# Performance work log

Measured on AMD Instinct MI355X. Metric: run time of the kernel, lower is better.

The kernel has to match this reference:

```python
import jax, jax.numpy as jnp
import numpy as np

B, C, H, E, V = 64, 200, 1024, 1024, 50257
NEG_INF = -100000.0


def setup_inputs() -> dict:
    key = jax.random.key(0)
    ks = jax.random.split(key, 16)
    p = 1.0 / np.sqrt(H)
    inp = {
        "input": jax.random.normal(ks[0], (B, 1, E), jnp.float32),
        "hidden": jax.random.normal(ks[1], (1, B, H), jnp.float32),
        "list_context_hidden": jax.random.normal(ks[2], (C, B, H), jnp.float32),
        "context_hiddens": jax.random.normal(ks[3], (B, C, H), jnp.float32),
        "topic_vector": jax.random.normal(ks[4], (B, 1, H), jnp.float32),
        "pad_matrix": jax.random.randint(ks[5], (B, C), 0, 2) > 0,
        # attention params
        "dyna_W": jax.random.normal(ks[6], (H, H), jnp.float32) * p,
        "dyna_U": jax.random.normal(ks[7], (H, H), jnp.float32) * p,
        "dyna_v": jax.random.normal(ks[8], (H, 1), jnp.float32) * p,
        # GRU params (torch layout: W_ih (3H, in), W_hh (3H, H))
        "W_ih": jax.random.normal(ks[9], (3 * H, 2 * H + E), jnp.float32) * p,
        "W_hh": jax.random.normal(ks[10], (3 * H, H), jnp.float32) * p,
        "b_ih": jax.random.normal(ks[11], (3 * H,), jnp.float32) * p,
        "b_hh": jax.random.normal(ks[12], (3 * H,), jnp.float32) * p,
        # output projection
        "W_out": jax.random.normal(ks[13], (V, H), jnp.float32) * p,
        "b_out": jax.random.normal(ks[14], (V,), jnp.float32) * p,
    }
    return inp


def _gru_step(x, h, W_ih, W_hh, b_ih, b_hh):
    # x: (B, in), h: (B, H) -> h': (B, H); torch GRUCell math
    gi = x @ W_ih.T + b_ih            # (B, 3H)
    gh = h @ W_hh.T + b_hh            # (B, 3H)
    r = jax.nn.sigmoid(gi[:, :H] + gh[:, :H])
    z = jax.nn.sigmoid(gi[:, H:2 * H] + gh[:, H:2 * H])
    n = jnp.tanh(gi[:, 2 * H:] + r * gh[:, 2 * H:])
    return (1.0 - z) * n + z * h


def reference(input, hidden, list_context_hidden, context_hiddens, topic_vector,
              pad_matrix, dyna_W, dyna_U, dyna_v, W_ih, W_hh, b_ih, b_hh,
              W_out, b_out):
    h0 = hidden[0]                                         # (B, H)
    # additive attention, vectorized over the C contexts
    q = h0 @ dyna_W                                        # (B, H)
    k = jnp.einsum('cbh,hk->cbk', list_context_hidden, dyna_U)  # (C, B, H)
    scores = jnp.tanh(q[None, :, :] + k) @ dyna_v          # (C, B, 1)
    scores = scores[..., 0].T                              # (B, C)
    scores = jnp.where(pad_matrix, NEG_INF, scores)
    attn = jax.nn.softmax(scores, axis=1)                  # (B, C)
    applied = jnp.einsum('bc,bch->bh', attn, context_hiddens)  # (B, H)
    # GRU over a single step
    x = jnp.concatenate([input[:, 0], topic_vector[:, 0], applied], axis=1)  # (B, E+2H)
    h_new = _gru_step(x, h0, W_ih, W_hh, b_ih, b_hh)       # (B, H)
    logits = h_new @ W_out.T + b_out                       # (B, V)
    out = jax.nn.log_softmax(logits, axis=1)
    return out, h_new[None]
```

## Files before the change

### kernel.cpp

```cpp
#include <hip/hip_runtime.h>
#include <hip/hip_bf16.h>
#include <math.h>

constexpr int Bsz = 64, Cctx = 200, Hdim = 1024, Vv = 50257;
constexpr float NEG_INF_V = -100000.0f;

typedef __attribute__((ext_vector_type(8))) short s16x8;
typedef __attribute__((ext_vector_type(4))) float fx4;
typedef unsigned int u32;

__device__ __forceinline__ unsigned short f2bf(float f) {
  unsigned int u = __builtin_bit_cast(unsigned int, f);
  unsigned int r = (u + 0x7fffu + ((u >> 16) & 1u)) >> 16;
  return (unsigned short)r;
}

__device__ __forceinline__ float fast_tanh(float x) {
  float e2 = __expf(2.f * x);
  return 1.f - 2.f / (e2 + 1.f);
}

__device__ __forceinline__ void gl_lds16(const unsigned short* g, unsigned short* l) {
  __builtin_amdgcn_global_load_lds(
      (const __attribute__((address_space(1))) u32*)g,
      (__attribute__((address_space(3))) u32*)l, 16, 0, 0);
}

__global__ __launch_bounds__(256)
void gemm_att(const unsigned short* __restrict__ Ab, const unsigned short* __restrict__ Bb,
              const float* __restrict__ qmat, const float* __restrict__ vvec,
              float* __restrict__ part_sc) {
  __shared__ unsigned short As[2][128 * 64];
  __shared__ unsigned short Bs[2][128 * 64];
  int f = blockIdx.x + blockIdx.y * 8;
  int xcd = f & 7, jj = f >> 3;
  int my = xcd + 8 * (jj % 13), mx = jj / 13;
  if (my >= 100) return;
  const int bm0 = my * 128, bn0 = mx * 128;
  const int tid = threadIdx.x, lane = tid & 63, wid = tid >> 6;
  const int wm0 = (wid >> 1) * 64, wn0 = (wid & 1) * 64;
  const int ar = lane & 15, q4 = lane >> 4;
  const int sw = ar & 7;

  auto STAGE = [&](int buf, int kt) {
    #pragma unroll
    for (int i = 0; i < 4; ++i) {
      int s = tid + i * 256;
      int row = s >> 3;
      int sc = ((s & 7) ^ (row & 7)) * 8;
      gl_lds16(&Ab[(size_t)(bm0 + row) * Hdim + kt + sc], &As[buf][s * 8]);
    }
    #pragma unroll
    for (int i = 0; i < 4; ++i) {
      int s = tid + i * 256;
      int row = s >> 3;
      int sc = ((s & 7) ^ (row & 7)) * 8;
      gl_lds16(&Bb[(size_t)(bn0 + row) * Hdim + kt + sc], &Bs[buf][s * 8]);
    }
  };

  fx4 acc[4][4] = {};
  STAGE(0, 0);
  __syncthreads();
  int buf = 0;

  for (int t = 0; t < 16; ++t) {
    if (t < 15) STAGE(buf ^ 1, (t + 1) * 64);
    asm volatile("" ::: "memory");
    #pragma unroll
    for (int kk = 0; kk < 2; ++kk) {
      s16x8 a[4], b[4];
      #pragma unroll
      for (int i = 0; i < 4; ++i)
        a[i] = *reinterpret_cast<const s16x8*>(
            &As[buf][(wm0 + i * 16 + ar) * 64 + (((kk * 4 + q4) ^ sw) * 8)]);
      #pragma unroll
      for (int j2 = 0; j2 < 4; ++j2)
        b[j2] = *reinterpret_cast<const s16x8*>(
            &Bs[buf][(wn0 + j2 * 16 + ar) * 64 + (((kk * 4 + q4) ^ sw) * 8)]);
      #pragma unroll
      for (int i = 0; i < 4; ++i)
        #pragma unroll
        for (int j2 = 0; j2 < 4; ++j2)
          acc[i][j2] = __builtin_amdgcn_mfma_f32_16x16x32_bf16(a[i], b[j2], acc[i][j2], 0, 0, 0);
    }
    __syncthreads();
    buf ^= 1;
  }

  const int rg = q4 * 4, cg = ar;
  #pragma unroll
  for (int i = 0; i < 4; ++i) {
    #pragma unroll
    for (int p = 0; p < 4; ++p) {
      int mg = bm0 + wm0 + i * 16 + rg + p;
      int brow = mg & 63;
      float rs = 0.f;
      #pragma unroll
      for (int j2 = 0; j2 < 4; ++j2) {
        int ng = bn0 + wn0 + j2 * 16 + cg;
        float t = fast_tanh(acc[i][j2][p] + qmat[brow * Hdim + ng]);
        rs += t * vvec[ng];
      }
      rs += __shfl_xor(rs, 1); rs += __shfl_xor(rs, 2);
      rs += __shfl_xor(rs, 4); rs += __shfl_xor(rs, 8);
      if (cg == 0) part_sc[mx * 12800 + brow * Cctx + (mg >> 6)] = rs;
    }
  }
}

__device__ __forceinline__ void stream_body(const unsigned short* ap, const float* bp,
                                            int stride, int extent, fx4 acc[4]) {
  float4 b0 = *reinterpret_cast<const float4*>(bp);
  float4 b1 = *reinterpret_cast<const float4*>(bp + 4);
  float4 b2 = *reinterpret_cast<const float4*>(bp + 32);
  float4 b3 = *reinterpret_cast<const float4*>(bp + 36);
  for (int kt = 0; kt < extent; kt += 64) {
    float4 c0 = b0, c1 = b1, c2 = b2, c3 = b3;
    if (kt + 64 < extent) {
      b0 = *reinterpret_cast<const float4*>(bp + kt + 64);
      b1 = *reinterpret_cast<const float4*>(bp + kt + 68);
      b2 = *reinterpret_cast<const float4*>(bp + kt + 96);
      b3 = *reinterpret_cast<const float4*>(bp + kt + 100);
    }
    s16x8 bf0, bf1;
    bf0[0] = (short)f2bf(c0.x); bf0[1] = (short)f2bf(c0.y);
    bf0[2] = (short)f2bf(c0.z); bf0[3] = (short)f2bf(c0.w);
    bf0[4] = (short)f2bf(c1.x); bf0[5] = (short)f2bf(c1.y);
    bf0[6] = (short)f2bf(c1.z); bf0[7] = (short)f2bf(c1.w);
    bf1[0] = (short)f2bf(c2.x); bf1[1] = (short)f2bf(c2.y);
    bf1[2] = (short)f2bf(c2.z); bf1[3] = (short)f2bf(c2.w);
    bf1[4] = (short)f2bf(c3.x); bf1[5] = (short)f2bf(c3.y);
    bf1[6] = (short)f2bf(c3.z); bf1[7] = (short)f2bf(c3.w);
    #pragma unroll
    for (int i = 0; i < 4; ++i) {
      s16x8 af = *reinterpret_cast<const s16x8*>(ap + (size_t)i * 16 * stride + kt);
      acc[i] = __builtin_amdgcn_mfma_f32_16x16x32_bf16(af, bf0, acc[i], 0, 0, 0);
    }
    #pragma unroll
    for (int i = 0; i < 4; ++i) {
      s16x8 af = *reinterpret_cast<const s16x8*>(ap + (size_t)i * 16 * stride + kt + 32);
      acc[i] = __builtin_amdgcn_mfma_f32_16x16x32_bf16(af, bf1, acc[i], 0, 0, 0);
    }
  }
}

template<int EPI>
__global__ __launch_bounds__(64)
void stream_gemm(const unsigned short* __restrict__ Ab,
                 const float* __restrict__ Bm, int N, int K,
                 const float* __restrict__ bias, float* __restrict__ Cout) {
  const int lane = threadIdx.x;
  const int n0 = blockIdx.x * 16;
  const int c = lane & 15, qq = lane >> 4;
  const int brow = min(n0 + c, N - 1);
  fx4 acc[4] = {};
  stream_body(Ab + (size_t)c * K + qq * 8, Bm + (size_t)brow * K + qq * 8, K, K, acc);
  const int n = n0 + c;
  if (n < N) {
    float bv = (EPI == 2) ? bias[n] : 0.f;
    #pragma unroll
    for (int i = 0; i < 4; ++i)
      #pragma unroll
      for (int p = 0; p < 4; ++p)
        Cout[(size_t)(i * 16 + qq * 4 + p) * N + n] = acc[i][p] + bv;
  }
}

__global__ __launch_bounds__(64)
void qgh_gemm(const unsigned short* __restrict__ h0b, const float* __restrict__ Wt,
              const float* __restrict__ Whh, const float* __restrict__ bhh,
              float* __restrict__ q, float* __restrict__ gh) {
  const int lane = threadIdx.x;
  const int gw = blockIdx.x;
  const bool isq = gw < 64;
  const int n0 = isq ? gw * 16 : (gw - 64) * 16;
  const int N = isq ? 1024 : 3072;
  const float* B = isq ? Wt : Whh;
  const int c = lane & 15, qq = lane >> 4;
  fx4 acc[4] = {};
  stream_body(h0b + (size_t)c * 1024 + qq * 8, B + (size_t)(n0 + c) * 1024 + qq * 8,
              1024, 1024, acc);
  const int n = n0 + c;
  float bv = isq ? 0.f : bhh[n];
  float* C = isq ? q : gh;
  #pragma unroll
  for (int i = 0; i < 4; ++i)
    #pragma unroll
    for (int p = 0; p < 4; ++p)
      C[(size_t)(i * 16 + qq * 4 + p) * N + n] = acc[i][p] + bv;
}

__global__ __launch_bounds__(64)
void gi_split(const unsigned short* __restrict__ xb, const float* __restrict__ Wih,
              float* __restrict__ part) {
  const int lane = threadIdx.x;
  const int t = blockIdx.x;
  const int w = blockIdx.y;
  const int c = lane & 15, qq = lane >> 4;
  constexpr int K = 3072, CH = 768;
  fx4 acc[4] = {};
  stream_body(xb + (size_t)c * K + w * CH + qq * 8,
              Wih + (size_t)(t * 16 + c) * K + w * CH + qq * 8, K, CH, acc);
  float* po = part + (size_t)w * 64 * 3072;
  const int n = t * 16 + c;
  #pragma unroll
  for (int i = 0; i < 4; ++i)
    #pragma unroll
    for (int p = 0; p < 4; ++p)
      po[(size_t)(i * 16 + qq * 4 + p) * 3072 + n] = acc[i][p];
}

__global__ __launch_bounds__(256)
void prep(const float* __restrict__ dW, const float* __restrict__ dU,
          const float* __restrict__ h0, float* __restrict__ Wt,
          unsigned short* __restrict__ ub, unsigned short* __restrict__ h0b) {
  const int z = blockIdx.z;
  const int tx = threadIdx.x & 31, ty = threadIdx.x >> 5;
  if (z < 2) {
    __shared__ float t[32][33];
    const float* in = z ? dU : dW;
    int bx = blockIdx.x * 32, by = blockIdx.y * 32;
    #pragma unroll
    for (int r = 0; r < 32; r += 8) t[ty + r][tx] = in[(size_t)(by + ty + r) * 1024 + bx + tx];
    __syncthreads();
    if (z == 0) {
      #pragma unroll
      for (int r = 0; r < 32; r += 8) Wt[(size_t)(bx + ty + r) * 1024 + by + tx] = t[tx][ty + r];
    } else {
      #pragma unroll
      for (int r = 0; r < 32; r += 8) ub[(size_t)(bx + ty + r) * 1024 + by + tx] = f2bf(t[tx][ty + r]);
    }
  } else {
    if (blockIdx.y) return;
    size_t i = (size_t)(blockIdx.x * 256 + threadIdx.x) * 8;
    float4 a = *reinterpret_cast<const float4*>(h0 + i);
    float4 b = *reinterpret_cast<const float4*>(h0 + i + 4);
    s16x8 h;
    h[0] = (short)f2bf(a.x); h[1] = (short)f2bf(a.y); h[2] = (short)f2bf(a.z); h[3] = (short)f2bf(a.w);
    h[4] = (short)f2bf(b.x); h[5] = (short)f2bf(b.y); h[6] = (short)f2bf(b.z); h[7] = (short)f2bf(b.w);
    *reinterpret_cast<s16x8*>(h0b + i) = h;
  }
}

__global__ void conv_bf16(const float* __restrict__ in, unsigned short* __restrict__ out) {
  size_t i = (size_t)(blockIdx.x * 256 + threadIdx.x) * 8;
  float4 a = *reinterpret_cast<const float4*>(in + i);
  float4 b = *reinterpret_cast<const float4*>(in + i + 4);
  s16x8 h;
  h[0] = (short)f2bf(a.x); h[1] = (short)f2bf(a.y); h[2] = (short)f2bf(a.z); h[3] = (short)f2bf(a.w);
  h[4] = (short)f2bf(b.x); h[5] = (short)f2bf(b.y); h[6] = (short)f2bf(b.z); h[7] = (short)f2bf(b.w);
  *reinterpret_cast<s16x8*>(out + i) = h;
}

__global__ __launch_bounds__(256)
void softmax_applied(const float* __restrict__ part_sc, const int* __restrict__ pad,
                     const float* __restrict__ ch, float* __restrict__ part) {
  const int g = blockIdx.x, b = blockIdx.y, t = threadIdx.x;
  const int lane = t & 63, w = t >> 6;
  __shared__ float at[256];
  __shared__ float red[8];
  float sv = 0.f, v = -3.4e38f;
  if (t < Cctx) {
    float s8 = 0.f;
    #pragma unroll
    for (int mx = 0; mx < 8; ++mx) s8 += part_sc[mx * 12800 + b * Cctx + t];
    sv = pad[b * Cctx + t] ? NEG_INF_V : s8;
    v = sv;
  }
  #pragma unroll
  for (int o = 1; o < 64; o <<= 1) v = fmaxf(v, __shfl_xor(v, o));
  if (lane == 0) red[w] = v;
  __syncthreads();
  float m = fmaxf(fmaxf(red[0], red[1]), fmaxf(red[2], red[3]));
  float e = (t < Cctx) ? expf(sv - m) : 0.f;
  float s = e;
  #pragma unroll
  for (int o = 1; o < 64; o <<= 1) s += __shfl_xor(s, o);
  if (lane == 0) red[4 + w] = s;
  __syncthreads();
  float tot = red[4] + red[5] + red[6] + red[7];
  at[t] = e / tot;
  __syncthreads();
  const int h = t * 4;
  float4 a4 = make_float4(0.f, 0.f, 0.f, 0.f);
  for (int c2 = g * 25; c2 < g * 25 + 25; ++c2) {
    float a = at[c2];
    float4 vv = *reinterpret_cast<const float4*>(&ch[((size_t)b * Cctx + c2) * Hdim + h]);
    a4.x += a * vv.x; a4.y += a * vv.y; a4.z += a * vv.z; a4.w += a * vv.w;
  }
  *reinterpret_cast<float4*>(&part[((size_t)b * 8 + g) * Hdim + h]) = a4;
}

__global__ void build_xb(const float* __restrict__ inp, const float* __restrict__ topic,
                         const float* __restrict__ part, unsigned short* __restrict__ xb) {
  int j = blockIdx.x * 256 + threadIdx.x;
  int b = blockIdx.y;
  float v;
  if (j < 1024) v = inp[b * 1024 + j];
  else if (j < 2048) v = topic[b * 1024 + (j - 1024)];
  else {
    const float* pp = &part[(size_t)b * 8 * Hdim + (j - 2048)];
    v = 0.f;
    #pragma unroll
    for (int g = 0; g < 8; ++g) v += pp[g * Hdim];
  }
  xb[(size_t)b * 3072 + j] = f2bf(v);
}

__global__ void gru_gate(const float* __restrict__ pgi, const float* __restrict__ bih,
                         const float* __restrict__ gh, const float* __restrict__ h0,
                         float* __restrict__ out_h, unsigned short* __restrict__ hnb) {
  int idx = blockIdx.x * 256 + threadIdx.x;
  int b = idx >> 10, j = idx & 1023;
  float gr = bih[j], gz = bih[1024 + j], gn = bih[2048 + j];
  const float* pb = pgi + (size_t)b * 3072;
  #pragma unroll
  for (int w = 0; w < 4; ++w) {
    const float* pw = pb + (size_t)w * 64 * 3072;
    gr += pw[j]; gz += pw[1024 + j]; gn += pw[2048 + j];
  }
  const float* ghb = gh + (size_t)b * 3072;
  float r = 1.f / (1.f + expf(-(gr + ghb[j])));
  float z = 1.f / (1.f + expf(-(gz + ghb[1024 + j])));
  float n = tanhf(gn + r * ghb[2048 + j]);
  float h = (1.f - z) * n + z * h0[idx];
  out_h[idx] = h;
  hnb[idx] = f2bf(h);
}

__global__ __launch_bounds__(256)
void lse_part(const float* __restrict__ out, float* __restrict__ pm, float* __restrict__ ps) {
  const int g = blockIdx.x, b = blockIdx.y, t = threadIdx.x;
  const int lane = t & 63, w = t >> 6;
  __shared__ float red[8];
  const float* row = out + (size_t)b * Vv;
  float m = -3.4e38f;
  for (int i = g * 256 + t; i < Vv; i += 2048) m = fmaxf(m, row[i]);
  #pragma unroll
  for (int o = 1; o < 64; o <<= 1) m = fmaxf(m, __shfl_xor(m, o));
  if (lane == 0) red[w] = m;
  __syncthreads();
  float mm = fmaxf(fmaxf(red[0], red[1]), fmaxf(red[2], red[3]));
  float s = 0.f;
  for (int i = g * 256 + t; i < Vv; i += 2048) s += expf(row[i] - mm);
  #pragma unroll
  for (int o = 1; o < 64; o <<= 1) s += __shfl_xor(s, o);
  if (lane == 0) red[4 + w] = s;
  __syncthreads();
  if (t == 0) {
    pm[b * 8 + g] = mm;
    ps[b * 8 + g] = red[4] + red[5] + red[6] + red[7];
  }
}

__global__ __launch_bounds__(256)
void lse_sub(float* __restrict__ out, const float* __restrict__ pm,
             const float* __restrict__ ps) {
  const int b = blockIdx.y;
  float M = -3.4e38f;
  #pragma unroll
  for (int g = 0; g < 8; ++g) M = fmaxf(M, pm[b * 8 + g]);
  float S = 0.f;
  #pragma unroll
  for (int g = 0; g < 8; ++g) S += ps[b * 8 + g] * expf(pm[b * 8 + g] - M);
  float lse = M + logf(S);
  int i = blockIdx.x * 256 + threadIdx.x;
  if (i < Vv) out[(size_t)b * Vv + i] -= lse;
}

extern "C" void kernel_launch(void* const* d_in, const int* in_sizes, int n_in,
                              void* d_out, int out_size, void* d_ws, size_t ws_size,
                              hipStream_t stream) {
  const float* input  = (const float*)d_in[0];
  const float* hidden = (const float*)d_in[1];
  const float* lch    = (const float*)d_in[2];
  const float* ch     = (const float*)d_in[3];
  const float* topic  = (const float*)d_in[4];
  const int*   pad    = (const int*)d_in[5];
  const float* dyna_W = (const float*)d_in[6];
  const float* dyna_U = (const float*)d_in[7];
  const float* dyna_v = (const float*)d_in[8];
  const float* W_ih   = (const float*)d_in[9];
  const float* W_hh   = (const float*)d_in[10];
  const float* b_ih   = (const float*)d_in[11];
  const float* b_hh   = (const float*)d_in[12];
  const float* W_out  = (const float*)d_in[13];
  const float* b_out  = (const float*)d_in[14];

  float* out   = (float*)d_out;
  float* out_h = out + (size_t)Bsz * Vv;

  float* p = (float*)d_ws;
  float* Wt      = p; p += 1024 * 1024;
  float* q       = p; p += Bsz * Hdim;
  float* part_sc = p; p += 8 * Bsz * Cctx;
  float* part_ap = p; p += Bsz * 8 * Hdim;
  float* gh      = p; p += Bsz * 3072;
  float* part_gi = p; p += 4 * Bsz * 3072;
  float* pm      = p; p += Bsz * 8;
  float* ps      = p; p += Bsz * 8;
  unsigned short* up = (unsigned short*)p;
  unsigned short* ub  = up; up += 1024 * 1024;
  unsigned short* lb  = up; up += (size_t)Cctx * Bsz * Hdim;
  unsigned short* h0b = up; up += Bsz * Hdim;
  unsigned short* hnb = up; up += Bsz * Hdim;
  unsigned short* xb  = up; up += Bsz * 3072;

  prep<<<dim3(32, 32, 3), 256, 0, stream>>>(dyna_W, dyna_U, hidden, Wt, ub, h0b);
  conv_bf16<<<(Cctx * Bsz * Hdim) / 2048, 256, 0, stream>>>(lch, lb);

  qgh_gemm<<<256, 64, 0, stream>>>(h0b, Wt, W_hh, b_hh, q, gh);

  gemm_att<<<dim3(8, 104), 256, 0, stream>>>(lb, ub, q, dyna_v, part_sc);

  softmax_applied<<<dim3(8, Bsz), 256, 0, stream>>>(part_sc, pad, ch, part_ap);
  build_xb<<<dim3(12, Bsz), 256, 0, stream>>>(input, topic, part_ap, xb);

  gi_split<<<dim3(192, 4), 64, 0, stream>>>(xb, W_ih, part_gi);

  gru_gate<<<(Bsz * Hdim) / 256, 256, 0, stream>>>(part_gi, b_ih, gh, hidden, out_h, hnb);

  stream_gemm<2><<<(Vv + 15) / 16, 64, 0, stream>>>(hnb, W_out, Vv, Hdim, b_out, out);

  lse_part<<<dim3(8, Bsz), 256, 0, stream>>>(out, pm, ps);
  lse_sub<<<dim3((Vv + 255) / 256, Bsz), 256, 0, stream>>>(out, pm, ps);
}
```

Measured before the change: 241.6 us.

## Keep 64-column dyna_U slice resident in LDS and stream A operand from global

The attention GEMM now makes each block load a full 64x1024 bf16 slice of dyna_U into LDS once (128 KB, XOR-swizzled). It then loops over M tiles, reading the list_context_hidden operand straight from global memory into registers with two-step prefetch. This replaces the double-buffered 128x128 tiling that re-staged both operands through LDS. Splitting N into 16 parts doubles the score partials, so the softmax kernel now sums 16 of them. Only 256 blocks run, each using 128 KB of LDS, so occupancy is low and A-operand latency may be poorly hidden.

```diff
diff --git a/kernel.cpp b/kernel.cpp
--- a/kernel.cpp
+++ b/kernel.cpp
@@ -20,91 +20,69 @@
   return 1.f - 2.f / (e2 + 1.f);
 }
 
-__device__ __forceinline__ void gl_lds16(const unsigned short* g, unsigned short* l) {
-  __builtin_amdgcn_global_load_lds(
-      (const __attribute__((address_space(1))) u32*)g,
-      (__attribute__((address_space(3))) u32*)l, 16, 0, 0);
-}
-
 __global__ __launch_bounds__(256)
 void gemm_att(const unsigned short* __restrict__ Ab, const unsigned short* __restrict__ Bb,
               const float* __restrict__ qmat, const float* __restrict__ vvec,
               float* __restrict__ part_sc) {
-  __shared__ unsigned short As[2][128 * 64];
-  __shared__ unsigned short Bs[2][128 * 64];
-  int f = blockIdx.x + blockIdx.y * 8;
-  int xcd = f & 7, jj = f >> 3;
-  int my = xcd + 8 * (jj % 13), mx = jj / 13;
-  if (my >= 100) return;
-  const int bm0 = my * 128, bn0 = mx * 128;
+  __shared__ unsigned short Bs[64 * 1024];
+  const int mc = blockIdx.x;
+  const int np = blockIdx.y;
+  const int n0 = np * 64;
   const int tid = threadIdx.x, lane = tid & 63, wid = tid >> 6;
-  const int wm0 = (wid >> 1) * 64, wn0 = (wid & 1) * 64;
   const int ar = lane & 15, q4 = lane >> 4;
-  const int sw = ar & 7;
-
-  auto STAGE = [&](int buf, int kt) {
-    #pragma unroll
-    for (int i = 0; i < 4; ++i) {
-      int s = tid + i * 256;
-      int row = s >> 3;
-      int sc = ((s & 7) ^ (row & 7)) * 8;
-      gl_lds16(&Ab[(size_t)(bm0 + row) * Hdim + kt + sc], &As[buf][s * 8]);
-    }
-    #pragma unroll
-    for (int i = 0; i < 4; ++i) {
-      int s = tid + i * 256;
-      int row = s >> 3;
-      int sc = ((s & 7) ^ (row & 7)) * 8;
-      gl_lds16(&Bb[(size_t)(bn0 + row) * Hdim + kt + sc], &Bs[buf][s * 8]);
-    }
-  };
-
-  fx4 acc[4][4] = {};
-  STAGE(0, 0);
-  __syncthreads();
-  int buf = 0;
-
-  for (int t = 0; t < 16; ++t) {
-    if (t < 15) STAGE(buf ^ 1, (t + 1) * 64);
-    asm volatile("" ::: "memory");
-    #pragma unroll
-    for (int kk = 0; kk < 2; ++kk) {
-      s16x8 a[4], b[4];
-      #pragma unroll
-      for (int i = 0; i < 4; ++i)
-        a[i] = *reinterpret_cast<const s16x8*>(
-            &As[buf][(wm0 + i * 16 + ar) * 64 + (((kk * 4 + q4) ^ sw) * 8)]);
-      #pragma unroll
-      for (int j2 = 0; j2 < 4; ++j2)
-        b[j2] = *reinterpret_cast<const s16x8*>(
-            &Bs[buf][(wn0 + j2 * 16 + ar) * 64 + (((kk * 4 + q4) ^ sw) * 8)]);
-      #pragma unroll
-      for (int i = 0; i < 4; ++i)
-        #pragma unroll
-        for (int j2 = 0; j2 < 4; ++j2)
-          acc[i][j2] = __builtin_amdgcn_mfma_f32_16x16x32_bf16(a[i], b[j2], acc[i][j2], 0, 0, 0);
-    }
-    __syncthreads();
-    buf ^= 1;
-  }
-
-  const int rg = q4 * 4, cg = ar;
-  #pragma unroll
-  for (int i = 0; i < 4; ++i) {
-    #pragma unroll
-    for (int p = 0; p < 4; ++p) {
-      int mg = bm0 + wm0 + i * 16 + rg + p;
-      int brow = mg & 63;
-      float rs = 0.f;
+
+  #pragma unroll
+  for (int it = 0; it < 32; ++it) {
+    int flat = tid + it * 256;
+    int row = flat >> 7, c16 = flat & 127;
+    s16x8 v = *reinterpret_cast<const s16x8*>(&Bb[(size_t)(n0 + row) * 1024 + c16 * 8]);
+    *reinterpret_cast<s16x8*>(&Bs[row * 1024 + ((c16 ^ (row & 7)) << 3)]) = v;
+  }
+  __syncthreads();
+
+  const int swz = ar & 7;
+
+  for (int mt = mc; mt < 100; mt += 16) {
+    const unsigned short* a0p = Ab + (size_t)(mt * 128 + wid * 32 + ar) * 1024 + q4 * 8;
+    const unsigned short* a1p = a0p + 16 * 1024;
+    fx4 acc[2][4] = {};
+    s16x8 c0 = *reinterpret_cast<const s16x8*>(a0p);
+    s16x8 c1 = *reinterpret_cast<const s16x8*>(a1p);
+    s16x8 n0a = *reinterpret_cast<const s16x8*>(a0p + 32);
+    s16x8 n1a = *reinterpret_cast<const s16x8*>(a1p + 32);
+    #pragma unroll 4
+    for (int k = 0; k < 32; ++k) {
+      s16x8 f0 = c0, f1 = c1;
+      c0 = n0a; c1 = n1a;
+      if (k + 2 < 32) {
+        n0a = *reinterpret_cast<const s16x8*>(a0p + (k + 2) * 32);
+        n1a = *reinterpret_cast<const s16x8*>(a1p + (k + 2) * 32);
+      }
       #pragma unroll
       for (int j2 = 0; j2 < 4; ++j2) {
-        int ng = bn0 + wn0 + j2 * 16 + cg;
-        float t = fast_tanh(acc[i][j2][p] + qmat[brow * Hdim + ng]);
-        rs += t * vvec[ng];
+        s16x8 b = *reinterpret_cast<const s16x8*>(
+            &Bs[(j2 * 16 + ar) * 1024 + (((k * 4 + q4) ^ swz) << 3)]);
+        acc[0][j2] = __builtin_amdgcn_mfma_f32_16x16x32_bf16(f0, b, acc[0][j2], 0, 0, 0);
+        acc[1][j2] = __builtin_amdgcn_mfma_f32_16x16x32_bf16(f1, b, acc[1][j2], 0, 0, 0);
       }
-      rs += __shfl_xor(rs, 1); rs += __shfl_xor(rs, 2);
-      rs += __shfl_xor(rs, 4); rs += __shfl_xor(rs, 8);
-      if (cg == 0) part_sc[mx * 12800 + brow * Cctx + (mg >> 6)] = rs;
+    }
+    #pragma unroll
+    for (int i = 0; i < 2; ++i) {
+      #pragma unroll
+      for (int p = 0; p < 4; ++p) {
+        int mg = mt * 128 + wid * 32 + i * 16 + q4 * 4 + p;
+        int brow = mg & 63;
+        float rs = 0.f;
+        #pragma unroll
+        for (int j2 = 0; j2 < 4; ++j2) {
+          int ng = n0 + j2 * 16 + ar;
+          float t = fast_tanh(acc[i][j2][p] + qmat[brow * Hdim + ng]);
+          rs += t * vvec[ng];
+        }
+        rs += __shfl_xor(rs, 1); rs += __shfl_xor(rs, 2);
+        rs += __shfl_xor(rs, 4); rs += __shfl_xor(rs, 8);
+        if (ar == 0) part_sc[np * 12800 + brow * Cctx + (mg >> 6)] = rs;
+      }
     }
   }
 }
@@ -264,7 +242,7 @@
   if (t < Cctx) {
     float s8 = 0.f;
     #pragma unroll
-    for (int mx = 0; mx < 8; ++mx) s8 += part_sc[mx * 12800 + b * Cctx + t];
+    for (int mx = 0; mx < 16; ++mx) s8 += part_sc[mx * 12800 + b * Cctx + t];
     sv = pad[b * Cctx + t] ? NEG_INF_V : s8;
     v = sv;
   }
@@ -394,7 +372,7 @@
   float* p = (float*)d_ws;
   float* Wt      = p; p += 1024 * 1024;
   float* q       = p; p += Bsz * Hdim;
-  float* part_sc = p; p += 8 * Bsz * Cctx;
+  float* part_sc = p; p += 16 * Bsz * Cctx;
   float* part_ap = p; p += Bsz * 8 * Hdim;
   float* gh      = p; p += Bsz * 3072;
   float* part_gi = p; p += 4 * Bsz * 3072;
@@ -412,7 +390,7 @@
 
   qgh_gemm<<<256, 64, 0, stream>>>(h0b, Wt, W_hh, b_hh, q, gh);
 
-  gemm_att<<<dim3(8, 104), 256, 0, stream>>>(lb, ub, q, dyna_v, part_sc);
+  gemm_att<<<dim3(16, 16), 256, 0, stream>>>(lb, ub, q, dyna_v, part_sc);
 
   softmax_applied<<<dim3(8, Bsz), 256, 0, stream>>>(part_sc, pad, ch, part_ap);
   build_xb<<<dim3(12, Bsz), 256, 0, stream>>>(input, topic, part_ap, xb);
```

After: 278.1 us. 15.1% more time.

## Use explicit vmcnt waits in attention GEMM and fuse log-softmax kernels

Applied to the files above, without the earlier changes.

The attention GEMM pipeline now waits with explicit s_waitcnt vmcnt counts and raw s_barrier calls instead of __syncthreads. This lets the prefetch of the next tile stay in flight while the current tile is consumed. The two log-sum-exp kernels are merged into one 1024-thread block per row that computes max, sum and the subtraction in a single launch. The merge drops a launch and the partial buffers, but leaves only 64 blocks to cover the whole GPU, which may underuse bandwidth.

```diff
diff --git a/kernel.cpp b/kernel.cpp
--- a/kernel.cpp
+++ b/kernel.cpp
@@ -61,12 +61,19 @@
 
   fx4 acc[4][4] = {};
   STAGE(0, 0);
-  __syncthreads();
+  asm volatile("s_waitcnt vmcnt(0)" ::: "memory");
+  __builtin_amdgcn_s_barrier();
   int buf = 0;
 
   for (int t = 0; t < 16; ++t) {
-    if (t < 15) STAGE(buf ^ 1, (t + 1) * 64);
-    asm volatile("" ::: "memory");
+    if (t < 15) {
+      STAGE(buf ^ 1, (t + 1) * 64);
+      asm volatile("s_waitcnt vmcnt(8)" ::: "memory");
+    } else {
+      asm volatile("s_waitcnt vmcnt(0)" ::: "memory");
+    }
+    __builtin_amdgcn_s_barrier();
+    __builtin_amdgcn_sched_barrier(0);
     #pragma unroll
     for (int kk = 0; kk < 2; ++kk) {
       s16x8 a[4], b[4];
@@ -84,7 +91,7 @@
         for (int j2 = 0; j2 < 4; ++j2)
           acc[i][j2] = __builtin_amdgcn_mfma_f32_16x16x32_bf16(a[i], b[j2], acc[i][j2], 0, 0, 0);
     }
-    __syncthreads();
+    __builtin_amdgcn_s_barrier();
     buf ^= 1;
   }
 
@@ -329,44 +336,32 @@
   hnb[idx] = f2bf(h);
 }
 
-__global__ __launch_bounds__(256)
-void lse_part(const float* __restrict__ out, float* __restrict__ pm, float* __restrict__ ps) {
-  const int g = blockIdx.x, b = blockIdx.y, t = threadIdx.x;
-  const int lane = t & 63, w = t >> 6;
-  __shared__ float red[8];
-  const float* row = out + (size_t)b * Vv;
+__global__ __launch_bounds__(1024)
+void lse_fused(float* __restrict__ out) {
+  const int b = blockIdx.x, t = threadIdx.x, lane = t & 63, w = t >> 6;
+  __shared__ float red[16];
+  float* row = out + (size_t)b * Vv;
   float m = -3.4e38f;
-  for (int i = g * 256 + t; i < Vv; i += 2048) m = fmaxf(m, row[i]);
+  for (int i = t; i < Vv; i += 1024) m = fmaxf(m, row[i]);
   #pragma unroll
   for (int o = 1; o < 64; o <<= 1) m = fmaxf(m, __shfl_xor(m, o));
   if (lane == 0) red[w] = m;
   __syncthreads();
-  float mm = fmaxf(fmaxf(red[0], red[1]), fmaxf(red[2], red[3]));
+  float mm = red[0];
+  #pragma unroll
+  for (int k = 1; k < 16; ++k) mm = fmaxf(mm, red[k]);
   float s = 0.f;
-  for (int i = g * 256 + t; i < Vv; i += 2048) s += expf(row[i] - mm);
+  for (int i = t; i < Vv; i += 1024) s += expf(row[i] - mm);
   #pragma unroll
   for (int o = 1; o < 64; o <<= 1) s += __shfl_xor(s, o);
-  if (lane == 0) red[4 + w] = s;
-  __syncthreads();
-  if (t == 0) {
-    pm[b * 8 + g] = mm;
-    ps[b * 8 + g] = red[4] + red[5] + red[6] + red[7];
-  }
-}
-
-__global__ __launch_bounds__(256)
-void lse_sub(float* __restrict__ out, const float* __restrict__ pm,
-             const float* __restrict__ ps) {
-  const int b = blockIdx.y;
-  float M = -3.4e38f;
-  #pragma unroll
-  for (int g = 0; g < 8; ++g) M = fmaxf(M, pm[b * 8 + g]);
-  float S = 0.f;
-  #pragma unroll
-  for (int g = 0; g < 8; ++g) S += ps[b * 8 + g] * expf(pm[b * 8 + g] - M);
-  float lse = M + logf(S);
-  int i = blockIdx.x * 256 + threadIdx.x;
-  if (i < Vv) out[(size_t)b * Vv + i] -= lse;
+  __syncthreads();
+  if (lane == 0) red[w] = s;
+  __syncthreads();
+  float ss = 0.f;
+  #pragma unroll
+  for (int k = 0; k < 16; ++k) ss += red[k];
+  float lse = mm + logf(ss);
+  for (int i = t; i < Vv; i += 1024) row[i] -= lse;
 }
 
 extern "C" void kernel_launch(void* const* d_in, const int* in_sizes, int n_in,
@@ -398,8 +393,6 @@
   float* part_ap = p; p += Bsz * 8 * Hdim;
   float* gh      = p; p += Bsz * 3072;
   float* part_gi = p; p += 4 * Bsz * 3072;
-  float* pm      = p; p += Bsz * 8;
-  float* ps      = p; p += Bsz * 8;
   unsigned short* up = (unsigned short*)p;
   unsigned short* ub  = up; up += 1024 * 1024;
   unsigned short* lb  = up; up += (size_t)Cctx * Bsz * Hdim;
@@ -423,6 +416,5 @@
 
   stream_gemm<2><<<(Vv + 15) / 16, 64, 0, stream>>>(hnb, W_out, Vv, Hdim, b_out, out);
 
-  lse_part<<<dim3(8, Bsz), 256, 0, stream>>>(out, pm, ps);
-  lse_sub<<<dim3((Vv + 255) / 256, Bsz), 256, 0, stream>>>(out, pm, ps);
-}
+  lse_fused<<<Bsz, 1024, 0, stream>>>(out);
+}
```

New measurement: 239.2 us. About the same (-1.0%).
